# Optimization experiments

Hardware: AMD Instinct MI355X
Metric: run time of the kernel (lower is better)

Reference implementation:

```python
import jax, jax.numpy as jnp
import numpy as np

NUM_CLASSES = 26
IGNORE_LABEL = 0
LAMBDA_SMOOTH = 1.0
EPSILON = 1e-05
# static indices of valid (non-ignored) classes
_VALID = np.array([c for c in range(NUM_CLASSES) if c != IGNORE_LABEL])


def setup_inputs() -> dict:
    key = jax.random.key(0)
    k1, k2, k3 = jax.random.split(key, 3)
    B, D, H, W = 1, 160, 192, 224
    fixed_label_map = jax.random.randint(k1, (B, D, H, W), 0, NUM_CLASSES, dtype=jnp.int32)
    warped_moving_label_map = jax.random.randint(k2, (B, D, H, W), 0, NUM_CLASSES, dtype=jnp.int32)
    vector_field = jax.random.normal(k3, (B, 3, D, H, W), dtype=jnp.float32)
    return {
        'fixed_label_map': fixed_label_map,
        'warped_moving_label_map': warped_moving_label_map,
        'vector_field': vector_field,
    }


def _soft_dice(fixed, moving):
    # Equivalent to one-hot expansion + sum over (B,D,H,W), but computed
    # directly from integer labels via histogram counts (single pass).
    f = fixed.reshape(-1)
    m = moving.reshape(-1)
    fixed_vol = jnp.bincount(f, length=NUM_CLASSES).astype(jnp.float32)
    moving_vol = jnp.bincount(m, length=NUM_CLASSES).astype(jnp.float32)
    # intersection[c] = #{voxels: f==c and m==c}
    inter = jnp.bincount(f, weights=(f == m).astype(jnp.float32), length=NUM_CLASSES)
    dice = (2.0 * inter + EPSILON) / (fixed_vol + moving_vol + EPSILON)
    return 1.0 - dice[_VALID].mean()


def _diffusion(vf):
    # vf: [B, 3, D, H, W]
    dz = vf[:, :, 1:, :, :] - vf[:, :, :-1, :, :]
    dy = vf[:, :, :, 1:, :] - vf[:, :, :, :-1, :]
    dx = vf[:, :, :, :, 1:] - vf[:, :, :, :, :-1]
    return (jnp.mean(dz * dz) + jnp.mean(dy * dy) + jnp.mean(dx * dx)) / 3.0


def reference(fixed_label_map, warped_moving_label_map, vector_field):
    similarity_loss = _soft_dice(fixed_label_map, warped_moving_label_map)
    smoothness_loss = _diffusion(vector_field)
    total_loss = similarity_loss + LAMBDA_SMOOTH * smoothness_loss
    return (total_loss, similarity_loss, smoothness_loss)
```

## Files before the change

kernel.cpp:

```cpp
#include <hip/hip_runtime.h>


namespace {
constexpr int NC    = 26;
constexpr int Dd    = 160, Hh = 192, Ww = 224;
constexpr int W4    = Ww / 4;
constexpr int PL4   = Hh * W4;
constexpr int N4L   = Dd * Hh * Ww / 4;
constexpr int JSTRIDE = 33;
constexpr int NBINS   = NC * JSTRIDE;
constexpr int HIST_BLOCKS = 840;
constexpr int HT          = HIST_BLOCKS * 256;
constexpr int SLAB    = 6;
constexpr int SLABS   = Hh / SLAB;
constexpr int SGRPS   = SLABS / 4;
constexpr int DCH     = 5;
constexpr int DCHUNKS = Dd / DCH;
constexpr int DIFF_BLOCKS = 3 * DCHUNKS * SGRPS;
}

__global__ void init_ws_kernel(unsigned int* __restrict__ joint,
                               double* __restrict__ sums) {
    int i = blockIdx.x * blockDim.x + threadIdx.x;
    if (i < NBINS) joint[i] = 0u;
    if (i < 3)     sums[i]  = 0.0;
}

__global__ __launch_bounds__(256, 4) void hist_kernel(
        const int4* __restrict__ f4,
        const int4* __restrict__ m4,
        unsigned int* __restrict__ gj) {
    __shared__ unsigned int h[NBINS];
    for (int i = threadIdx.x; i < NBINS; i += 256) h[i] = 0u;
    __syncthreads();

    const int g = blockIdx.x * 256 + threadIdx.x;
    int4 a0 = f4[g];
    int4 a1 = f4[g + HT];
    int4 a2 = f4[g + 2 * HT];
    int4 a3 = f4[g + 3 * HT];
    int4 a4 = f4[g + 4 * HT];
    int4 a5 = f4[g + 5 * HT];
    int4 a6 = f4[g + 6 * HT];
    int4 a7 = f4[g + 7 * HT];
    int4 b0 = m4[g];
    int4 b1 = m4[g + HT];
    int4 b2 = m4[g + 2 * HT];
    int4 b3 = m4[g + 3 * HT];
    int4 b4 = m4[g + 4 * HT];
    int4 b5 = m4[g + 5 * HT];
    int4 b6 = m4[g + 6 * HT];
    int4 b7 = m4[g + 7 * HT];

#define JACC(A, B)                                   \
    atomicAdd(&h[(A).x * JSTRIDE + (B).x], 1u);      \
    atomicAdd(&h[(A).y * JSTRIDE + (B).y], 1u);      \
    atomicAdd(&h[(A).z * JSTRIDE + (B).z], 1u);      \
    atomicAdd(&h[(A).w * JSTRIDE + (B).w], 1u);
    JACC(a0, b0) JACC(a1, b1) JACC(a2, b2) JACC(a3, b3)
    JACC(a4, b4) JACC(a5, b5) JACC(a6, b6) JACC(a7, b7)
#undef JACC

    __syncthreads();
    for (int i = threadIdx.x; i < NBINS; i += 256) {
        unsigned int v = h[i];
        if (v) atomicAdd(&gj[i], v);
    }
}

__global__ __launch_bounds__(256, 3) void diff_kernel(
        const float4* __restrict__ v4,
        double* __restrict__ gs) {
    const int lane = threadIdx.x & 63;
    const int wid  = threadIdx.x >> 6;
    const int b    = blockIdx.x;
    const int c      = b / (DCHUNKS * SGRPS);
    const int rem    = b % (DCHUNKS * SGRPS);
    const int dchunk = rem / SGRPS;
    const int sgrp   = rem % SGRPS;
    const int slab   = sgrp * 4 + wid;
    const int h0     = slab * SLAB;
    const int d0     = dchunk * DCH;
    const bool al    = (lane < W4);
    const bool hv    = (h0 + SLAB < Hh);
    const int  l     = al ? lane : (W4 - 1);

    size_t cur = ((size_t)(c * Dd + d0) * Hh + h0) * W4 + l;

    float4 p0 = v4[cur];
    float4 p1 = v4[cur + W4];
    float4 p2 = v4[cur + 2 * W4];
    float4 p3 = v4[cur + 3 * W4];
    float4 p4 = v4[cur + 4 * W4];
    float4 p5 = v4[cur + 5 * W4];

    float sx = 0.f, sy = 0.f, sz = 0.f;
    const int haloOff = (hv ? SLAB : SLAB - 1) * W4;

    for (int k = 0; k < DCH; ++k) {
        const int d = d0 + k;
        const bool dzv = (d < Dd - 1);
        float4 hl = v4[cur + haloOff];
        float4 n0 = p0, n1 = p1, n2 = p2, n3 = p3, n4 = p4, n5 = p5;
        if (dzv) {
            const size_t nb = cur + PL4;
            n0 = v4[nb];
            n1 = v4[nb + W4];
            n2 = v4[nb + 2 * W4];
            n3 = v4[nb + 3 * W4];
            n4 = v4[nb + 4 * W4];
            n5 = v4[nb + 5 * W4];
        }

#define DX(P)                                                                  \
        {                                                                      \
            float d1 = (P).y - (P).x, d2 = (P).z - (P).y, d3 = (P).w - (P).z;  \
            sx += d1 * d1 + d2 * d2 + d3 * d3;                                 \
            float nx = __shfl_down((P).x, 1);                                  \
            float d4 = nx - (P).w;                                             \
            sx += (lane < W4 - 1) ? d4 * d4 : 0.f;                             \
        }
        DX(p0) DX(p1) DX(p2) DX(p3) DX(p4) DX(p5)
#undef DX
#define DY(A, B)                                                               \
        {                                                                      \
            float e0 = (B).x - (A).x, e1 = (B).y - (A).y;                      \
            float e2 = (B).z - (A).z, e3 = (B).w - (A).w;                      \
            sy += e0 * e0 + e1 * e1 + e2 * e2 + e3 * e3;                       \
        }
        DY(p0, p1) DY(p1, p2) DY(p2, p3) DY(p3, p4) DY(p4, p5)
        if (hv) DY(p5, hl)
#undef DY
        if (dzv) {
#define DZ(A, B)                                                               \
            {                                                                  \
                float e0 = (B).x - (A).x, e1 = (B).y - (A).y;                  \
                float e2 = (B).z - (A).z, e3 = (B).w - (A).w;                  \
                sz += e0 * e0 + e1 * e1 + e2 * e2 + e3 * e3;                   \
            }
            DZ(p0, n0) DZ(p1, n1) DZ(p2, n2) DZ(p3, n3) DZ(p4, n4) DZ(p5, n5)
#undef DZ
        }
        p0 = n0; p1 = n1; p2 = n2; p3 = n3; p4 = n4; p5 = n5;
        cur += PL4;
    }

    if (!al) { sx = 0.f; sy = 0.f; sz = 0.f; }

    #pragma unroll
    for (int off = 32; off > 0; off >>= 1) {
        sx += __shfl_down(sx, off);
        sy += __shfl_down(sy, off);
        sz += __shfl_down(sz, off);
    }
    __shared__ float px[4], py[4], pz[4];
    if (lane == 0) { px[wid] = sx; py[wid] = sy; pz[wid] = sz; }
    __syncthreads();
    if (threadIdx.x == 0) {
        atomicAdd(&gs[0], (double)(px[0] + px[1] + px[2] + px[3]));
        atomicAdd(&gs[1], (double)(py[0] + py[1] + py[2] + py[3]));
        atomicAdd(&gs[2], (double)(pz[0] + pz[1] + pz[2] + pz[3]));
    }
}

__global__ void finalize_kernel(const unsigned int* __restrict__ gj,
                                const double* __restrict__ gs,
                                float* __restrict__ out) {
    int lane = threadIdx.x & 63;
    float term = 0.f;
    if (lane >= 1 && lane < NC) {
        float fv = 0.f, mv = 0.f;
        #pragma unroll
        for (int m = 0; m < NC; ++m) fv += (float)gj[lane * JSTRIDE + m];
        #pragma unroll
        for (int f = 0; f < NC; ++f) mv += (float)gj[f * JSTRIDE + lane];
        float iv = (float)gj[lane * JSTRIDE + lane];
        term = (2.f * iv + 1e-5f) / (fv + mv + 1e-5f);
    }
    #pragma unroll
    for (int off = 32; off > 0; off >>= 1) term += __shfl_down(term, off);
    if (threadIdx.x == 0 && blockIdx.x == 0) {
        float sim = 1.f - term * (1.f / 25.f);
        double mdx = gs[0] / ((double)3 * Dd * Hh * (Ww - 1));
        double mdy = gs[1] / ((double)3 * Dd * (Hh - 1) * Ww);
        double mdz = gs[2] / ((double)3 * (Dd - 1) * Hh * Ww);
        float smooth = (float)((mdx + mdy + mdz) / 3.0);
        out[0] = sim + smooth;
        out[1] = sim;
        out[2] = smooth;
    }
}

extern "C" void kernel_launch(void* const* d_in, const int* in_sizes, int n_in,
                              void* d_out, int out_size, void* d_ws, size_t ws_size,
                              hipStream_t stream) {
    const int*   fl = (const int*)d_in[0];
    const int*   ml = (const int*)d_in[1];
    const float* vf = (const float*)d_in[2];
    float* out = (float*)d_out;

    unsigned int* joint = (unsigned int*)d_ws;
    double*       sums  = (double*)((char*)d_ws + 3584);

    init_ws_kernel<<<1, 1024, 0, stream>>>(joint, sums);
    hist_kernel<<<HIST_BLOCKS, 256, 0, stream>>>((const int4*)fl, (const int4*)ml, joint);
    diff_kernel<<<DIFF_BLOCKS, 256, 0, stream>>>((const float4*)vf, sums);
    finalize_kernel<<<1, 64, 0, stream>>>(joint, sums, out);
}
```

Measured before the change: 205.0 us.

## Stage histogram loads via global_load_lds and share diffusion halos through LDS

The histogram kernel now loops over 7 chunks per block and stages label tiles straight into shared memory with the global_load_lds builtin, replacing the register-held 8-way unrolled loads. The diffusion kernel shrinks slabs to 3 rows and processes 10 depth planes per block. Adjacent waves now take their y-halo row from the neighbouring wave's data in LDS instead of reloading it from global memory, so only the last wave loads a halo. The cost is two block barriers per depth step and per histogram iteration, less memory-level parallelism per thread, and reliance on the LDS-direct load layout being correct.

```diff
diff --git a/kernel.cpp b/kernel.cpp
--- a/kernel.cpp
+++ b/kernel.cpp
@@ -9,15 +9,18 @@
 constexpr int N4L   = Dd * Hh * Ww / 4;
 constexpr int JSTRIDE = 33;
 constexpr int NBINS   = NC * JSTRIDE;
-constexpr int HIST_BLOCKS = 840;
-constexpr int HT          = HIST_BLOCKS * 256;
-constexpr int SLAB    = 6;
+constexpr int HIST_BLOCKS = 960;
+constexpr int HIST_ITERS  = 7;
+constexpr int SLAB    = 3;
 constexpr int SLABS   = Hh / SLAB;
 constexpr int SGRPS   = SLABS / 4;
-constexpr int DCH     = 5;
+constexpr int DCH     = 10;
 constexpr int DCHUNKS = Dd / DCH;
 constexpr int DIFF_BLOCKS = 3 * DCHUNKS * SGRPS;
 }
+
+typedef __attribute__((address_space(1))) const void* gva_t;
+typedef __attribute__((address_space(3))) void* lva_t;
 
 __global__ void init_ws_kernel(unsigned int* __restrict__ joint,
                                double* __restrict__ sums) {
@@ -26,42 +29,34 @@
     if (i < 3)     sums[i]  = 0.0;
 }
 
-__global__ __launch_bounds__(256, 4) void hist_kernel(
+__global__ __launch_bounds__(256) void hist_kernel(
         const int4* __restrict__ f4,
         const int4* __restrict__ m4,
         unsigned int* __restrict__ gj) {
+    __shared__ int4 sf[256];
+    __shared__ int4 sm[256];
     __shared__ unsigned int h[NBINS];
     for (int i = threadIdx.x; i < NBINS; i += 256) h[i] = 0u;
-    __syncthreads();
-
-    const int g = blockIdx.x * 256 + threadIdx.x;
-    int4 a0 = f4[g];
-    int4 a1 = f4[g + HT];
-    int4 a2 = f4[g + 2 * HT];
-    int4 a3 = f4[g + 3 * HT];
-    int4 a4 = f4[g + 4 * HT];
-    int4 a5 = f4[g + 5 * HT];
-    int4 a6 = f4[g + 6 * HT];
-    int4 a7 = f4[g + 7 * HT];
-    int4 b0 = m4[g];
-    int4 b1 = m4[g + HT];
-    int4 b2 = m4[g + 2 * HT];
-    int4 b3 = m4[g + 3 * HT];
-    int4 b4 = m4[g + 4 * HT];
-    int4 b5 = m4[g + 5 * HT];
-    int4 b6 = m4[g + 6 * HT];
-    int4 b7 = m4[g + 7 * HT];
-
-#define JACC(A, B)                                   \
-    atomicAdd(&h[(A).x * JSTRIDE + (B).x], 1u);      \
-    atomicAdd(&h[(A).y * JSTRIDE + (B).y], 1u);      \
-    atomicAdd(&h[(A).z * JSTRIDE + (B).z], 1u);      \
-    atomicAdd(&h[(A).w * JSTRIDE + (B).w], 1u);
-    JACC(a0, b0) JACC(a1, b1) JACC(a2, b2) JACC(a3, b3)
-    JACC(a4, b4) JACC(a5, b5) JACC(a6, b6) JACC(a7, b7)
-#undef JACC
-
-    __syncthreads();
+
+    const int wid = threadIdx.x >> 6;
+    int base = blockIdx.x * (HIST_ITERS * 256);
+
+    for (int it = 0; it < HIST_ITERS; ++it) {
+        __builtin_amdgcn_global_load_lds((gva_t)(f4 + base + threadIdx.x),
+                                         (lva_t)(sf + wid * 64), 16, 0, 0);
+        __builtin_amdgcn_global_load_lds((gva_t)(m4 + base + threadIdx.x),
+                                         (lva_t)(sm + wid * 64), 16, 0, 0);
+        __syncthreads();
+        int4 a = sf[threadIdx.x];
+        int4 b = sm[threadIdx.x];
+        atomicAdd(&h[a.x * JSTRIDE + b.x], 1u);
+        atomicAdd(&h[a.y * JSTRIDE + b.y], 1u);
+        atomicAdd(&h[a.z * JSTRIDE + b.z], 1u);
+        atomicAdd(&h[a.w * JSTRIDE + b.w], 1u);
+        __syncthreads();
+        base += 256;
+    }
+
     for (int i = threadIdx.x; i < NBINS; i += 256) {
         unsigned int v = h[i];
         if (v) atomicAdd(&gj[i], v);
@@ -71,6 +66,9 @@
 __global__ __launch_bounds__(256, 3) void diff_kernel(
         const float4* __restrict__ v4,
         double* __restrict__ gs) {
+    __shared__ float4 halo[4][W4];
+    __shared__ float px[4], py[4], pz[4];
+
     const int lane = threadIdx.x & 63;
     const int wid  = threadIdx.x >> 6;
     const int b    = blockIdx.x;
@@ -82,7 +80,7 @@
     const int h0     = slab * SLAB;
     const int d0     = dchunk * DCH;
     const bool al    = (lane < W4);
-    const bool hv    = (h0 + SLAB < Hh);
+    const bool hv    = (slab < SLABS - 1);
     const int  l     = al ? lane : (W4 - 1);
 
     size_t cur = ((size_t)(c * Dd + d0) * Hh + h0) * W4 + l;
@@ -90,27 +88,22 @@
     float4 p0 = v4[cur];
     float4 p1 = v4[cur + W4];
     float4 p2 = v4[cur + 2 * W4];
-    float4 p3 = v4[cur + 3 * W4];
-    float4 p4 = v4[cur + 4 * W4];
-    float4 p5 = v4[cur + 5 * W4];
 
     float sx = 0.f, sy = 0.f, sz = 0.f;
-    const int haloOff = (hv ? SLAB : SLAB - 1) * W4;
 
     for (int k = 0; k < DCH; ++k) {
-        const int d = d0 + k;
-        const bool dzv = (d < Dd - 1);
-        float4 hl = v4[cur + haloOff];
-        float4 n0 = p0, n1 = p1, n2 = p2, n3 = p3, n4 = p4, n5 = p5;
+        const bool dzv = (d0 + k < Dd - 1);
+        if (al) halo[wid][lane] = p0;
+        float4 hl = p2;
+        if (wid == 3 && hv) hl = v4[cur + SLAB * W4];
+        float4 n0 = p0, n1 = p1, n2 = p2;
         if (dzv) {
-            const size_t nb = cur + PL4;
-            n0 = v4[nb];
-            n1 = v4[nb + W4];
-            n2 = v4[nb + 2 * W4];
-            n3 = v4[nb + 3 * W4];
-            n4 = v4[nb + 4 * W4];
-            n5 = v4[nb + 5 * W4];
-        }
+            n0 = v4[cur + PL4];
+            n1 = v4[cur + PL4 + W4];
+            n2 = v4[cur + PL4 + 2 * W4];
+        }
+        __syncthreads();
+        if (wid < 3) hl = halo[wid + 1][l];
 
 #define DX(P)                                                                  \
         {                                                                      \
@@ -120,7 +113,7 @@
             float d4 = nx - (P).w;                                             \
             sx += (lane < W4 - 1) ? d4 * d4 : 0.f;                             \
         }
-        DX(p0) DX(p1) DX(p2) DX(p3) DX(p4) DX(p5)
+        DX(p0) DX(p1) DX(p2)
 #undef DX
 #define DY(A, B)                                                               \
         {                                                                      \
@@ -128,8 +121,8 @@
             float e2 = (B).z - (A).z, e3 = (B).w - (A).w;                      \
             sy += e0 * e0 + e1 * e1 + e2 * e2 + e3 * e3;                       \
         }
-        DY(p0, p1) DY(p1, p2) DY(p2, p3) DY(p3, p4) DY(p4, p5)
-        if (hv) DY(p5, hl)
+        DY(p0, p1) DY(p1, p2)
+        if (hv) DY(p2, hl)
 #undef DY
         if (dzv) {
 #define DZ(A, B)                                                               \
@@ -138,10 +131,11 @@
                 float e2 = (B).z - (A).z, e3 = (B).w - (A).w;                  \
                 sz += e0 * e0 + e1 * e1 + e2 * e2 + e3 * e3;                   \
             }
-            DZ(p0, n0) DZ(p1, n1) DZ(p2, n2) DZ(p3, n3) DZ(p4, n4) DZ(p5, n5)
+            DZ(p0, n0) DZ(p1, n1) DZ(p2, n2)
 #undef DZ
         }
-        p0 = n0; p1 = n1; p2 = n2; p3 = n3; p4 = n4; p5 = n5;
+        __syncthreads();
+        p0 = n0; p1 = n1; p2 = n2;
         cur += PL4;
     }
 
@@ -153,7 +147,6 @@
         sy += __shfl_down(sy, off);
         sz += __shfl_down(sz, off);
     }
-    __shared__ float px[4], py[4], pz[4];
     if (lane == 0) { px[wid] = sx; py[wid] = sy; pz[wid] = sz; }
     __syncthreads();
     if (threadIdx.x == 0) {
```

Result: no change. 207.8 us (+1.3%).
